# Kernel optimization log

Hardware: AMD Instinct MI355X
Metric: run time of the kernel (lower is better)

The kernel has to match this reference:

```python
import jax, jax.numpy as jnp
import numpy as np

DIM_HIDDEN = 512
NUM_CLASSES = 100
LAMBDA_C = 1.0
POOL = 8  # Maha_distance pools the feature dim into 8 groups


def setup_inputs() -> dict:
    key = jax.random.key(0)
    k1, k2, k3 = jax.random.split(key, 3)
    B = 1024
    hidden = jax.random.normal(k1, (B, DIM_HIDDEN), dtype=jnp.float32)
    feature_center = jax.random.normal(k2, (NUM_CLASSES, DIM_HIDDEN), dtype=jnp.float32)
    y = jax.random.randint(k3, (B,), 0, NUM_CLASSES, dtype=jnp.int64 if jax.config.jax_enable_x64 else jnp.int32)
    return {"hidden": hidden, "feature_center": feature_center, "y": y}


def _batch_cov(points):
    # points: [B, N, D] -> [B, D, D]; matches torch batch_cov (sum of outer products / (N-1))
    B, N, D = points.shape
    diffs = points - points.mean(axis=1, keepdims=True)
    return jnp.einsum('bnd,bne->bde', diffs, diffs) / (N - 1)


def _maha_distance(X, Y):
    # X, Y: [bs, a, b]
    bs, a, b = X.shape
    X = X.reshape(bs, a, POOL, b // POOL).mean(axis=3)  # [bs, a, 8]
    Y = Y.reshape(bs, a, POOL, b // POOL).mean(axis=3)
    X = X / (jnp.linalg.norm(X, axis=2, keepdims=True) + 1e-6)
    Y = Y / (jnp.linalg.norm(Y, axis=2, keepdims=True) + 1e-6)
    XY = jnp.concatenate([X, Y], axis=1)  # [bs, 2a, 8]
    bcov = _batch_cov(XY)                 # [bs, 8, 8]
    pinv_cov = jnp.linalg.pinv(bcov, hermitian=True)
    X_Y = X - Y                           # [bs, a, 8]
    m_dis = jnp.einsum('bad,bde,bae->ba', X_Y, pinv_cov, X_Y)
    return jnp.sqrt(m_dis)


def reference(hidden, feature_center, y):
    B = hidden.shape[0]
    one_y = jax.nn.one_hot(y, NUM_CLASSES, dtype=hidden.dtype)
    center = jnp.broadcast_to(feature_center[None, :, :], (B, NUM_CLASSES, DIM_HIDDEN))
    c_feature = jnp.broadcast_to(hidden[:, None, :], (B, NUM_CLASSES, DIM_HIDDEN))
    dis = _maha_distance(c_feature, center)  # [B, C]
    intra_maha = jnp.sum(dis * one_y, axis=1)
    inter_maha = jnp.sum(dis * (1.0 - one_y), axis=1) / (NUM_CLASSES - 1)
    loss = intra_maha + LAMBDA_C * (-inter_maha)
    return loss.mean()
```

## Files before the change

kernel.cpp:

```cpp
#include <hip/hip_runtime.h>
#include <math.h>


#define DIMH 512
#define NC   100
#define PG   8
#define GS   64
#define RPB  4

__global__ __launch_bounds__(256) void ccl_main_kernel(
    const float* __restrict__ hidden,
    const float* __restrict__ fc,
    const int*   __restrict__ y,
    double* __restrict__ partials,
    int B)
{
    __shared__ float  cn[NC][PG];
    __shared__ float  cbarS[PG];
    __shared__ float  SinvS[64];
    __shared__ float  Spart[RPB][64];
    __shared__ double wpart[RPB];

    const int tid  = threadIdx.x;
    const int lane = tid & 63;
    const int wave = tid >> 6;
    const int b    = blockIdx.x * RPB + wave;

    float4 h0 = make_float4(0.f, 0.f, 0.f, 0.f);
    float4 h1 = make_float4(0.f, 0.f, 0.f, 0.f);
    int yt = -1;
    if (b < B) {
        const float4* hrow = reinterpret_cast<const float4*>(hidden + (size_t)b * DIMH) + lane * 2;
        h0 = hrow[0];
        h1 = hrow[1];
        yt = y[b];
    }

    for (int c = wave; c < NC; c += RPB) {
        const float4* row = reinterpret_cast<const float4*>(fc + (size_t)c * DIMH) + lane * 2;
        float4 a = row[0];
        float4 d = row[1];
        float s = a.x + a.y + a.z + a.w + d.x + d.y + d.z + d.w;
        s += __shfl_xor(s, 1);
        s += __shfl_xor(s, 2);
        s += __shfl_xor(s, 4);
        if ((lane & 7) == 0) cn[c][lane >> 3] = s * (1.0f / GS);
    }
    __syncthreads();

    if (tid < NC) {
        float v[PG];
        float n2 = 0.0f;
#pragma unroll
        for (int g = 0; g < PG; ++g) { v[g] = cn[tid][g]; n2 += v[g] * v[g]; }
        float inv = 1.0f / (sqrtf(n2) + 1e-6f);
#pragma unroll
        for (int g = 0; g < PG; ++g) cn[tid][g] = v[g] * inv;
    }
    __syncthreads();

    if (wave == 1) {
        const int g = lane & 7, t = lane >> 3;
        float s = 0.0f;
        for (int c = t; c < NC; c += 8) s += cn[c][g];
        s += __shfl_xor(s, 8);
        s += __shfl_xor(s, 16);
        s += __shfl_xor(s, 32);
        if (t == 0) cbarS[g] = s * (1.0f / NC);
    }
    {
        const int i = lane >> 3, j = lane & 7;
        const int c0 = wave * (NC / RPB);
        float s = 0.0f;
        for (int c = c0; c < c0 + NC / RPB; ++c) s += cn[c][i] * cn[c][j];
        Spart[wave][lane] = s;
    }
    __syncthreads();

    if (wave == 0) {
        const int i = lane >> 3, j = lane & 7;
        float a = Spart[0][lane] + Spart[1][lane] + Spart[2][lane] + Spart[3][lane]
                - (float)NC * cbarS[i] * cbarS[j];
        float binv = (i == j) ? 1.0f : 0.0f;
#pragma unroll
        for (int k = 0; k < 8; ++k) {
            float akk = __shfl(a,    k * 8 + k);
            float aik = __shfl(a,    i * 8 + k);
            float akj = __shfl(a,    k * 8 + j);
            float bkj = __shfl(binv, k * 8 + j);
            float r = 1.0f / akk;
            if (i == k) { a *= r;            binv *= r; }
            else        { float f = aik * r; a -= f * akj; binv -= f * bkj; }
        }
        SinvS[lane] = binv;
    }
    __syncthreads();

    double loss_b = 0.0;
    if (b < B) {
        float s = h0.x + h0.y + h0.z + h0.w + h1.x + h1.y + h1.z + h1.w;
        s += __shfl_xor(s, 1);
        s += __shfl_xor(s, 2);
        s += __shfl_xor(s, 4);

        float hn[PG];
        float n2 = 0.0f;
#pragma unroll
        for (int g = 0; g < PG; ++g) {
            hn[g] = __shfl(s, g << 3) * (1.0f / GS);
            n2 += hn[g] * hn[g];
        }
        float inv = 1.0f / (sqrtf(n2) + 1e-6f);
#pragma unroll
        for (int g = 0; g < PG; ++g) hn[g] *= inv;

        float u[PG], w[PG];
#pragma unroll
        for (int g = 0; g < PG; ++g) u[g] = hn[g] - cbarS[g];
        float uw = 0.0f;
#pragma unroll
        for (int ii = 0; ii < PG; ++ii) {
            float t = 0.0f;
#pragma unroll
            for (int jj = 0; jj < PG; ++jj) t += SinvS[ii * 8 + jj] * u[jj];
            w[ii] = t;
            uw += u[ii] * t;
        }
        const float coef = 50.0f / (1.0f + 50.0f * uw);

        float sumd = 0.0f, disy = 0.0f;
        for (int c = lane; c < NC; c += 64) {
            float v[PG];
#pragma unroll
            for (int g = 0; g < PG; ++g) v[g] = hn[g] - cn[c][g];
            float q1 = 0.0f, q2 = 0.0f;
#pragma unroll
            for (int ii = 0; ii < PG; ++ii) {
                float t = 0.0f;
#pragma unroll
                for (int jj = 0; jj < PG; ++jj) t += SinvS[ii * 8 + jj] * v[jj];
                q1 += v[ii] * t;
                q2 += v[ii] * w[ii];
            }
            float m = 199.0f * (q1 - coef * q2 * q2);
            float d = sqrtf(fmaxf(m, 0.0f));
            sumd += d;
            if (c == yt) disy = d;
        }
#pragma unroll
        for (int off = 1; off < 64; off <<= 1) {
            sumd += __shfl_xor(sumd, off);
            disy += __shfl_xor(disy, off);
        }
        loss_b = (double)disy - (double)(sumd - disy) * (1.0 / 99.0);
    }

    if (lane == 0) wpart[wave] = loss_b;
    __syncthreads();

    if (tid == 0)
        partials[blockIdx.x] = wpart[0] + wpart[1] + wpart[2] + wpart[3];
}

__global__ __launch_bounds__(256) void ccl_finalize_kernel(
    const double* __restrict__ partials, float* __restrict__ out, int n, int B)
{
    __shared__ double sh[4];
    const int tid = threadIdx.x, lane = tid & 63, wave = tid >> 6;
    double v = (tid < n) ? partials[tid] : 0.0;
#pragma unroll
    for (int off = 1; off < 64; off <<= 1) v += __shfl_xor(v, off);
    if (lane == 0) sh[wave] = v;
    __syncthreads();
    if (tid == 0) out[0] = (float)((sh[0] + sh[1] + sh[2] + sh[3]) / (double)B);
}

extern "C" void kernel_launch(void* const* d_in, const int* in_sizes, int n_in,
                              void* d_out, int out_size, void* d_ws, size_t ws_size,
                              hipStream_t stream)
{
    const float* hidden = (const float*)d_in[0];
    const float* fc     = (const float*)d_in[1];
    const int*   y      = (const int*)d_in[2];
    float*       out    = (float*)d_out;

    const int B = in_sizes[0] / DIMH;
    const int nblocks = (B + RPB - 1) / RPB;

    double* partials = (double*)d_ws;

    ccl_main_kernel<<<nblocks, 256, 0, stream>>>(hidden, fc, y, partials, B);
    ccl_finalize_kernel<<<1, 256, 0, stream>>>(partials, out, nblocks, B);
}
```

Measured before the change: 70.54 us.

## Precompute class statistics once and expand quadratic forms per class

Moves center normalization, covariance inversion and per-class products Sinv·c into a single-block stats kernel, instead of every block redoing them. The loss kernel then expands the quadratic forms algebraically, so each class costs one 8-wide dot product rather than an 8x8 matrix-vector product. The separate finalize kernel is replaced by an atomic accumulate with a last-block counter. The trade-off is a serial single-block kernel in front of the main one, double-precision atomics, and extra rounding from the expanded quadratic form.

```diff
diff --git a/kernel.cpp b/kernel.cpp
--- a/kernel.cpp
+++ b/kernel.cpp
@@ -8,33 +8,30 @@
 #define GS   64
 #define RPB  4
 
-__global__ __launch_bounds__(256) void ccl_main_kernel(
-    const float* __restrict__ hidden,
+#define WS_ACCUM   0
+#define WS_COUNTER 8
+#define WS_SINV    16
+#define WS_CBAR    272
+#define WS_MBAR    304
+#define WS_MC      336
+
+__global__ __launch_bounds__(256) void ccl_stats_kernel(
     const float* __restrict__ fc,
-    const int*   __restrict__ y,
-    double* __restrict__ partials,
-    int B)
+    double* __restrict__ accum,
+    unsigned* __restrict__ counter,
+    float* __restrict__ SinvG,
+    float* __restrict__ cbarG,
+    float* __restrict__ mbarG,
+    float* __restrict__ McG)
 {
-    __shared__ float  cn[NC][PG];
-    __shared__ float  cbarS[PG];
-    __shared__ float  SinvS[64];
-    __shared__ float  Spart[RPB][64];
-    __shared__ double wpart[RPB];
+    __shared__ float cn[NC][9];
+    __shared__ float cbarS[PG];
+    __shared__ float SinvS[64];
+    __shared__ float Spart[RPB][64];
 
     const int tid  = threadIdx.x;
     const int lane = tid & 63;
     const int wave = tid >> 6;
-    const int b    = blockIdx.x * RPB + wave;
-
-    float4 h0 = make_float4(0.f, 0.f, 0.f, 0.f);
-    float4 h1 = make_float4(0.f, 0.f, 0.f, 0.f);
-    int yt = -1;
-    if (b < B) {
-        const float4* hrow = reinterpret_cast<const float4*>(hidden + (size_t)b * DIMH) + lane * 2;
-        h0 = hrow[0];
-        h1 = hrow[1];
-        yt = y[b];
-    }
 
     for (int c = wave; c < NC; c += RPB) {
         const float4* row = reinterpret_cast<const float4*>(fc + (size_t)c * DIMH) + lane * 2;
@@ -96,6 +93,76 @@
     }
     __syncthreads();
 
+    if (tid < NC) {
+        float m[PG];
+        float q = 0.0f, s = 0.0f;
+#pragma unroll
+        for (int ii = 0; ii < PG; ++ii) {
+            float t = 0.0f;
+#pragma unroll
+            for (int jj = 0; jj < PG; ++jj) t += SinvS[ii * 8 + jj] * cn[tid][jj];
+            m[ii] = t;
+            q += t * cn[tid][ii];
+            s += t * cbarS[ii];
+        }
+        float* dst = McG + tid * 10;
+#pragma unroll
+        for (int ii = 0; ii < PG; ++ii) dst[ii] = m[ii];
+        dst[8] = q;
+        dst[9] = s;
+    }
+    if (tid >= 248) {
+        const int ii = tid - 248;
+        float t = 0.0f;
+#pragma unroll
+        for (int jj = 0; jj < PG; ++jj) t += SinvS[ii * 8 + jj] * cbarS[jj];
+        mbarG[ii] = t;
+    }
+    if (tid < 64) SinvG[tid] = SinvS[tid];
+    if (tid >= 240 && tid < 248) cbarG[tid - 240] = cbarS[tid - 240];
+    if (tid == 0) { *accum = 0.0; *counter = 0u; }
+}
+
+__global__ __launch_bounds__(256) void ccl_loss_kernel(
+    const float* __restrict__ hidden,
+    const int*   __restrict__ y,
+    const float* __restrict__ SinvG,
+    const float* __restrict__ cbarG,
+    const float* __restrict__ mbarG,
+    const float* __restrict__ McG,
+    double* __restrict__ accum,
+    unsigned* __restrict__ counter,
+    float* __restrict__ out,
+    int B, int nblocks)
+{
+    __shared__ float  Mc[NC][11];
+    __shared__ float  SinvS[64];
+    __shared__ float  cbarS[PG];
+    __shared__ float  mbarS[PG];
+    __shared__ double wpart[RPB];
+
+    const int tid  = threadIdx.x;
+    const int lane = tid & 63;
+    const int wave = tid >> 6;
+    const int b    = blockIdx.x * RPB + wave;
+
+    float4 h0 = make_float4(0.f, 0.f, 0.f, 0.f);
+    float4 h1 = make_float4(0.f, 0.f, 0.f, 0.f);
+    int yt = -1;
+    if (b < B) {
+        const float4* hrow = reinterpret_cast<const float4*>(hidden + (size_t)b * DIMH) + lane * 2;
+        h0 = hrow[0];
+        h1 = hrow[1];
+        yt = y[b];
+    }
+
+    if (tid < 64) SinvS[tid] = SinvG[tid];
+    if (tid >= 64 && tid < 72)  cbarS[tid - 64] = cbarG[tid - 64];
+    if (tid >= 72 && tid < 80)  mbarS[tid - 72] = mbarG[tid - 72];
+    for (int idx = tid; idx < NC * 10; idx += 256)
+        Mc[idx / 10][idx % 10] = McG[idx];
+    __syncthreads();
+
     double loss_b = 0.0;
     if (b < B) {
         float s = h0.x + h0.y + h0.z + h0.w + h1.x + h1.y + h1.z + h1.w;
@@ -114,36 +181,34 @@
 #pragma unroll
         for (int g = 0; g < PG; ++g) hn[g] *= inv;
 
-        float u[PG], w[PG];
-#pragma unroll
-        for (int g = 0; g < PG; ++g) u[g] = hn[g] - cbarS[g];
-        float uw = 0.0f;
+        float z[PG];
+        float alpha = 0.0f;
 #pragma unroll
         for (int ii = 0; ii < PG; ++ii) {
             float t = 0.0f;
 #pragma unroll
-            for (int jj = 0; jj < PG; ++jj) t += SinvS[ii * 8 + jj] * u[jj];
-            w[ii] = t;
-            uw += u[ii] * t;
+            for (int jj = 0; jj < PG; ++jj) t += SinvS[ii * 8 + jj] * hn[jj];
+            z[ii] = t;
+            alpha += t * hn[ii];
+        }
+        float beta = 0.0f, uw = 0.0f;
+#pragma unroll
+        for (int ii = 0; ii < PG; ++ii) {
+            float wv = z[ii] - mbarS[ii];
+            beta += wv * hn[ii];
+            uw   += wv * (hn[ii] - cbarS[ii]);
         }
         const float coef = 50.0f / (1.0f + 50.0f * uw);
 
         float sumd = 0.0f, disy = 0.0f;
         for (int c = lane; c < NC; c += 64) {
-            float v[PG];
-#pragma unroll
-            for (int g = 0; g < PG; ++g) v[g] = hn[g] - cn[c][g];
-            float q1 = 0.0f, q2 = 0.0f;
-#pragma unroll
-            for (int ii = 0; ii < PG; ++ii) {
-                float t = 0.0f;
-#pragma unroll
-                for (int jj = 0; jj < PG; ++jj) t += SinvS[ii * 8 + jj] * v[jj];
-                q1 += v[ii] * t;
-                q2 += v[ii] * w[ii];
-            }
-            float m = 199.0f * (q1 - coef * q2 * q2);
-            float d = sqrtf(fmaxf(m, 0.0f));
+            float hm = 0.0f;
+#pragma unroll
+            for (int g = 0; g < PG; ++g) hm += hn[g] * Mc[c][g];
+            float vSv = alpha - 2.0f * hm + Mc[c][8];
+            float vw  = beta - hm + Mc[c][9];
+            float m   = 199.0f * (vSv - coef * vw * vw);
+            float d   = sqrtf(fmaxf(m, 0.0f));
             sumd += d;
             if (c == yt) disy = d;
         }
@@ -158,21 +223,16 @@
     if (lane == 0) wpart[wave] = loss_b;
     __syncthreads();
 
-    if (tid == 0)
-        partials[blockIdx.x] = wpart[0] + wpart[1] + wpart[2] + wpart[3];
-}
-
-__global__ __launch_bounds__(256) void ccl_finalize_kernel(
-    const double* __restrict__ partials, float* __restrict__ out, int n, int B)
-{
-    __shared__ double sh[4];
-    const int tid = threadIdx.x, lane = tid & 63, wave = tid >> 6;
-    double v = (tid < n) ? partials[tid] : 0.0;
-#pragma unroll
-    for (int off = 1; off < 64; off <<= 1) v += __shfl_xor(v, off);
-    if (lane == 0) sh[wave] = v;
-    __syncthreads();
-    if (tid == 0) out[0] = (float)((sh[0] + sh[1] + sh[2] + sh[3]) / (double)B);
+    if (tid == 0) {
+        double t = wpart[0] + wpart[1] + wpart[2] + wpart[3];
+        atomicAdd(accum, t);
+        __threadfence();
+        unsigned old = atomicAdd(counter, 1u);
+        if (old == (unsigned)(nblocks - 1)) {
+            double v = atomicAdd(accum, 0.0);
+            out[0] = (float)(v / (double)B);
+        }
+    }
 }
 
 extern "C" void kernel_launch(void* const* d_in, const int* in_sizes, int n_in,
@@ -187,8 +247,16 @@
     const int B = in_sizes[0] / DIMH;
     const int nblocks = (B + RPB - 1) / RPB;
 
-    double* partials = (double*)d_ws;
-
-    ccl_main_kernel<<<nblocks, 256, 0, stream>>>(hidden, fc, y, partials, B);
-    ccl_finalize_kernel<<<1, 256, 0, stream>>>(partials, out, nblocks, B);
+    char* ws = (char*)d_ws;
+    double*   accum   = (double*)(ws + WS_ACCUM);
+    unsigned* counter = (unsigned*)(ws + WS_COUNTER);
+    float*    SinvG   = (float*)(ws + WS_SINV);
+    float*    cbarG   = (float*)(ws + WS_CBAR);
+    float*    mbarG   = (float*)(ws + WS_MBAR);
+    float*    McG     = (float*)(ws + WS_MC);
+
+    ccl_stats_kernel<<<1, 256, 0, stream>>>(fc, accum, counter,
+                                            SinvG, cbarG, mbarG, McG);
+    ccl_loss_kernel<<<nblocks, 256, 0, stream>>>(hidden, y, SinvG, cbarG, mbarG, McG,
+                                                 accum, counter, out, B, nblocks);
 }
```

After: 79.51 us. 1.13x slower.
